# Kernel tuning notes

Measured on AMD Instinct MI355X. Metric: run time of the kernel, lower is better.

## Reference

```python
import jax, jax.numpy as jnp
import numpy as np

B, N, X_DIM, Y_DIM, H_DIM, R_DIM = 64, 512, 128, 128, 4096, 1024


def setup_inputs() -> dict:
    key = jax.random.key(0)
    ks = jax.random.split(key, 10)
    x = jax.random.normal(ks[0], (B, N, X_DIM), dtype=jnp.float32)
    y = jax.random.normal(ks[1], (B, N, Y_DIM), dtype=jnp.float32)
    # per-sample context lengths in [1, N]; prefix mask guarantees >=1 True per row
    lengths = jax.random.randint(ks[2], (B,), 1, N + 1)
    mask = (jnp.arange(N)[None, :] < lengths[:, None])  # [B, N] bool
    d_in = X_DIM + Y_DIM
    s1 = 1.0 / np.sqrt(d_in)
    s2 = 1.0 / np.sqrt(H_DIM)
    W1 = jax.random.uniform(ks[3], (d_in, H_DIM), jnp.float32, -s1, s1)
    b1 = jax.random.uniform(ks[4], (H_DIM,), jnp.float32, -s1, s1)
    W2 = jax.random.uniform(ks[5], (H_DIM, H_DIM), jnp.float32, -s2, s2)
    b2 = jax.random.uniform(ks[6], (H_DIM,), jnp.float32, -s2, s2)
    W3 = jax.random.uniform(ks[7], (H_DIM, R_DIM), jnp.float32, -s2, s2)
    b3 = jax.random.uniform(ks[8], (R_DIM,), jnp.float32, -s2, s2)
    return {"x": x, "y": y, "mask": mask,
            "W1": W1, "b1": b1, "W2": W2, "b2": b2, "W3": W3, "b3": b3}


def reference(x, y, mask, W1, b1, W2, b2, W3, b3):
    # Dense equivalent of gather -> MLP -> scatter_mean by batch id:
    # the MLP is pointwise over tokens, so applying it densely and taking a
    # masked mean over the point dim gives identical math to the ragged path.
    nn_in = jnp.concatenate([x, y], axis=-1)          # [B, N, x+y]
    h = jax.nn.relu(jnp.einsum('bnd,dh->bnh', nn_in, W1) + b1)
    h = jax.nn.relu(jnp.einsum('bnh,hk->bnk', h, W2) + b2)
    r = jnp.einsum('bnk,kr->bnr', h, W3) + b3          # [B, N, r_dim]
    m = mask.astype(r.dtype)[..., None]                # [B, N, 1]
    counts = jnp.maximum(m.sum(axis=1), 1.0)           # [B, 1]
    r_aggr = (r * m).sum(axis=1) / counts              # [B, r_dim]
    return r_aggr
```

## Files before the change

kernel.cpp:

```cpp
#include <hip/hip_runtime.h>


using u16 = unsigned short;
using u8 = unsigned char;
typedef float f32x4 __attribute__((ext_vector_type(4)));
typedef short s16x8 __attribute__((ext_vector_type(8)));
typedef int i32x4 __attribute__((ext_vector_type(4)));

__device__ __forceinline__ u16 f2bf(float f) {
  union { float f; unsigned u; } v; v.f = f;
  unsigned r = (v.u + 0x7fffu + ((v.u >> 16) & 1u)) >> 16;
  return (u16)r;
}


__global__ void count_k(const int* __restrict__ mask, int* __restrict__ lens) {
  int b = blockIdx.x, l = threadIdx.x;
  const int4* row = (const int4*)(mask + (size_t)b * 512);
  int4 v0 = row[l];
  int4 v1 = row[l + 64];
  int s = v0.x + v0.y + v0.z + v0.w + v1.x + v1.y + v1.z + v1.w;
  #pragma unroll
  for (int o = 32; o; o >>= 1) s += __shfl_down(s, o);
  if (l == 0) lens[b] = s;
}

__global__ void meta_k(const int* __restrict__ lens, int* __restrict__ meta) {
  if (threadIdx.x == 0) {
    int acc = 0; meta[0] = 0;
    for (int b = 0; b < 64; ++b) { acc += lens[b]; meta[b + 1] = acc; }
    meta[65] = acc;
    meta[66] = (acc + 127) >> 7;
  }
}

__global__ void tok2b_k(const int* __restrict__ meta, int* __restrict__ tok2b) {
  int i = blockIdx.x * 256 + threadIdx.x;
  int total = meta[65];
  int b = 64;
  if (i < total) {
    int lo = 0, hi = 64;
    while (hi - lo > 1) { int mid = (lo + hi) >> 1; if (meta[mid] <= i) lo = mid; else hi = mid; }
    b = lo;
  }
  tok2b[i] = b;
}

__global__ void build_a(const float* __restrict__ x, const float* __restrict__ y,
                        const int* __restrict__ meta, const int* __restrict__ tok2b,
                        u16* __restrict__ A) {
  int i4 = blockIdx.x * 256 + threadIdx.x;
  int e = i4 * 4;
  int m = e >> 8, c = e & 255;
  int total = meta[65];
  ushort4 o = {0, 0, 0, 0};
  if (m < total) {
    int b = tok2b[m], t = m - meta[b];
    const float* src = (c < 128) ? x + ((size_t)b * 512 + t) * 128 + c
                                 : y + ((size_t)b * 512 + t) * 128 + (c - 128);
    float4 v = *(const float4*)src;
    o.x = f2bf(v.x); o.y = f2bf(v.y); o.z = f2bf(v.z); o.w = f2bf(v.w);
  }
  *(ushort4*)&A[e] = o;
}

__global__ void pack_k(const float* __restrict__ W, u16* __restrict__ P,
                       int N, int NKB) {
  long c = (long)blockIdx.x * 256 + threadIdx.x;
  int lane = c & 63; long r = c >> 6;
  int s = r & 1; int j = (r >> 1) & 3; int wn = (r >> 3) & 1;
  long q = r >> 4;
  int ktb = (int)(q % NKB), nt = (int)(q / NKB);
  int k = ktb * 64 + s * 32 + (lane >> 4) * 8;
  int n = nt * 128 + wn * 64 + j * 16 + (lane & 15);
  ushort o[8];
  #pragma unroll
  for (int e = 0; e < 8; ++e) o[e] = f2bf(W[(size_t)(k + e) * N + n]);
  *(uint4*)&P[c * 8] = *(uint4*)o;
}

__global__ void colmax_k(const float* __restrict__ W, float* __restrict__ cmax) {
  int n = blockIdx.x * 256 + threadIdx.x;
  int k0 = blockIdx.y * 128;
  float m = 0.f;
  for (int k = k0; k < k0 + 128; ++k)
    m = fmaxf(m, fabsf(W[(size_t)k * 4096 + n]));
  atomicMax((int*)&cmax[n], __float_as_int(m));
}

__global__ void pack8_k(const float* __restrict__ W, const float* __restrict__ cmax,
                        char* __restrict__ P) {
  long c = (long)blockIdx.x * 256 + threadIdx.x;
  int lane = c & 63; long r = c >> 6;
  int j = r & 3; int wn = (r >> 2) & 1; long q = r >> 3;
  int ktb = (int)(q & 63), nt = (int)(q >> 6);
  int k = ktb * 64 + (lane >> 4) * 16;
  int n = nt * 128 + wn * 64 + j * 16 + (lane & 15);
  float rw = 127.0f / fmaxf(cmax[n], 1e-20f);
  char o[16];
  #pragma unroll
  for (int e = 0; e < 16; ++e) {
    int v = __float2int_rn(W[(size_t)(k + e) * 4096 + n] * rw);
    v = v > 127 ? 127 : (v < -127 ? -127 : v);
    o[e] = (char)v;
  }
  *(uint4*)&P[c * 16] = *(const uint4*)o;
}

__global__ void sn_k(const float* __restrict__ S, const int* __restrict__ lens,
                     u16* __restrict__ Sn) {
  int i4 = blockIdx.x * 256 + threadIdx.x;
  int e = i4 * 4;
  int m = e >> 12;
  float inv = (m < 64) ? (1.0f / (float)lens[m]) : 0.0f;
  float4 v = *(const float4*)(S + e);
  ushort4 o;
  o.x = f2bf(v.x * inv); o.y = f2bf(v.y * inv);
  o.z = f2bf(v.z * inv); o.w = f2bf(v.w * inv);
  *(ushort4*)&Sn[e] = o;
}

template <int MODE>
__global__ __launch_bounds__(256, 3) void gemm_k(
    const void* __restrict__ Av, int lda, const void* __restrict__ BPv,
    const float* __restrict__ bias, const float* __restrict__ cmax,
    u8* __restrict__ Hout, float* __restrict__ Sout, float* __restrict__ Fout,
    const int* __restrict__ meta, const int* __restrict__ tok2b,
    int K, int Nld, int tile0, int tile_cap) {
  constexpr bool A8 = (MODE == 1);
  constexpr int BK = A8 ? 128 : 64;
  __shared__ union {
    u16 a16[2][128 * 64];
    u8  a8[2][128 * 128];
    u8  outT8[128 * 128];
  } sm;

  const int tid = threadIdx.x;
  const int wave = tid >> 6;
  const int lane = tid & 63;
  const int wm = wave >> 1, wn = wave & 1;
  const int quad = lane >> 4, l15 = lane & 15;
  const int NKB = K >> 6;

  int nslots;
  if constexpr (MODE < 2) {
    int tc = meta[66] - tile0;
    tc = tc < 0 ? 0 : (tc > tile_cap ? tile_cap : tc);
    nslots = tc * 32;
  } else {
    nslots = gridDim.x;
  }

  for (int slot = blockIdx.x; slot < nslots; slot += gridDim.x) {
    int mt, n0, k0, kend;
    if constexpr (MODE < 2) {
      mt = slot >> 5; n0 = (slot & 31) << 7; k0 = 0; kend = K;
    } else {
      mt = 0; n0 = slot << 7; k0 = blockIdx.y * 512; kend = k0 + 512;
    }

    f32x4 accf[4][4];
    i32x4 acci[4][4];
    #pragma unroll
    for (int i = 0; i < 4; i++)
      #pragma unroll
      for (int j = 0; j < 4; j++) {
        if constexpr (A8) acci[i][j] = (i32x4){0, 0, 0, 0};
        else accf[i][j] = (f32x4){0.f, 0.f, 0.f, 0.f};
      }

    const u8* ag8[4];
    const u16* ag16[4];
    if constexpr (A8) {
      #pragma unroll
      for (int il = 0; il < 4; ++il) {
        int ci = (wave * 4 + il) * 64 + lane;
        int m = ci >> 3, c = (ci & 7) ^ (m & 7);
        ag8[il] = (const u8*)Av + (size_t)(mt * 128 + m) * lda + c * 16;
      }
    } else {
      #pragma unroll
      for (int il = 0; il < 4; ++il) {
        int ci = (wave * 4 + il) * 64 + lane;
        int m = ci >> 3, c = (ci & 7) ^ (m & 7);
        ag16[il] = (const u16*)Av + (size_t)(mt * 128 + m) * lda + c * 8;
      }
    }
    const u16* bw = nullptr;
    const u8* bw8 = nullptr;
    if constexpr (A8)
      bw8 = (const u8*)BPv + (size_t)(n0 >> 7) * NKB * 8192 + wn * 4096 + lane * 16;
    else
      bw = (const u16*)BPv + (size_t)(n0 >> 7) * NKB * 8192 + wn * 4096 + lane * 8;

    s16x8 breg0[8], breg1[8];
    i32x4 breg8_0[8], breg8_1[8];

    auto stageA = [&](int kt, int buf) {
      if constexpr (A8) {
        #pragma unroll
        for (int il = 0; il < 4; ++il)
          __builtin_amdgcn_global_load_lds(
              (const __attribute__((address_space(1))) void*)(ag8[il] + kt),
              (__attribute__((address_space(3))) void*)(&sm.a8[buf][(wave * 4 + il) * 1024]),
              16, 0, 0);
      } else {
        #pragma unroll
        for (int il = 0; il < 4; ++il)
          __builtin_amdgcn_global_load_lds(
              (const __attribute__((address_space(1))) void*)(ag16[il] + kt),
              (__attribute__((address_space(3))) void*)(&sm.a16[buf][(wave * 4 + il) * 512]),
              16, 0, 0);
      }
    };
    auto loadB = [&](int kt, int which) {
      if constexpr (A8) {
        i32x4* dst = which ? breg8_1 : breg8_0;
        const u8* p = bw8 + (size_t)(kt >> 6) * 8192;
        #pragma unroll
        for (int s = 0; s < 2; s++)
          #pragma unroll
          for (int j = 0; j < 4; j++)
            dst[s * 4 + j] = *(const i32x4*)(p + s * 8192 + j * 1024);
      } else {
        s16x8* dst = which ? breg1 : breg0;
        const u16* p = bw + (size_t)(kt >> 6) * 8192;
        #pragma unroll
        for (int j = 0; j < 4; j++)
          #pragma unroll
          for (int s = 0; s < 2; s++)
            dst[j * 2 + s] = *(const s16x8*)(p + j * 1024 + s * 512);
      }
    };
    auto compute = [&](int buf) {
      if constexpr (A8) {
        const i32x4* br = buf ? breg8_1 : breg8_0;
        #pragma unroll
        for (int s = 0; s < 2; ++s) {
          #pragma unroll
          for (int i = 0; i < 4; i++) {
            int m = wm * 64 + i * 16 + l15;
            int c = (s * 4 + quad) ^ (m & 7);
            i32x4 a = *(const i32x4*)&sm.a8[buf][(m * 8 + c) * 16];
            #pragma unroll
            for (int j = 0; j < 4; j++)
              acci[i][j] = __builtin_amdgcn_mfma_i32_16x16x64_i8(
                  a, br[s * 4 + j], acci[i][j], 0, 0, 0);
          }
        }
      } else {
        const s16x8* br = buf ? breg1 : breg0;
        #pragma unroll
        for (int s = 0; s < 2; ++s) {
          s16x8 af[4];
          #pragma unroll
          for (int i = 0; i < 4; i++) {
            int m = wm * 64 + i * 16 + l15;
            int c = (s * 4 + quad) ^ (m & 7);
            af[i] = *(const s16x8*)&sm.a16[buf][(m * 8 + c) * 8];
          }
          #pragma unroll
          for (int i = 0; i < 4; i++)
            #pragma unroll
            for (int j = 0; j < 4; j++)
              accf[i][j] = __builtin_amdgcn_mfma_f32_16x16x32_bf16(
                  af[i], br[j * 2 + s], accf[i][j], 0, 0, 0);
        }
      }
    };

    stageA(k0, 0);
    loadB(k0, 0);
    const int NP = (kend - k0) / BK;
    for (int t = 0; t < NP; t += 2) {
      int kt = k0 + t * BK;
      __builtin_amdgcn_s_waitcnt(0x0F78);
      __builtin_amdgcn_s_barrier();
      stageA(kt + BK, 1);
      __builtin_amdgcn_sched_barrier(0);
      loadB(kt + BK, 1);
      compute(0);
      __builtin_amdgcn_s_waitcnt(0x0F78);
      __builtin_amdgcn_s_barrier();
      if (t + 2 < NP) {
        stageA(kt + 2 * BK, 0);
        __builtin_amdgcn_sched_barrier(0);
        loadB(kt + 2 * BK, 0);
      }
      compute(1);
    }
    __syncthreads();

    if constexpr (MODE == 0) {
      float bb[4];
      #pragma unroll
      for (int j = 0; j < 4; j++) bb[j] = bias[n0 + wn * 64 + j * 16 + l15];
      #pragma unroll
      for (int i = 0; i < 4; i++)
        #pragma unroll
        for (int j = 0; j < 4; j++) {
          int col = wn * 64 + j * 16 + l15;
          #pragma unroll
          for (int r = 0; r < 4; r++) {
            int row = wm * 64 + i * 16 + quad * 4 + r;
            float v = accf[i][j][r] + bb[j];
            v = v > 0.f ? v : 0.f;
            int qv = (int)(v * 32.0f + 0.5f);
            if (qv > 127) qv = 127;
            sm.outT8[row * 128 + col] = (u8)qv;
          }
        }
      __syncthreads();
      #pragma unroll
      for (int u = 0; u < 4; ++u) {
        int e = u * 256 + tid;
        int row = e >> 3, c16 = (e & 7) * 16;
        *(uint4*)&Hout[(size_t)(mt * 128 + row) * Nld + n0 + c16] =
            *(const uint4*)&sm.outT8[row * 128 + c16];
      }
      __syncthreads();
    } else if constexpr (MODE == 1) {
      float bb[4], sc[4];
      #pragma unroll
      for (int j = 0; j < 4; j++) {
        int col_ = n0 + wn * 64 + j * 16 + l15;
        bb[j] = bias[col_];
        sc[j] = cmax[col_] * (1.0f / (127.0f * 32.0f));
      }
      int tb[16];
      const int gbase = tile0 * 128 + mt * 128 + wm * 64 + quad * 4;
      #pragma unroll
      for (int i = 0; i < 4; i++)
        #pragma unroll
        for (int r = 0; r < 4; r++) tb[i * 4 + r] = tok2b[gbase + i * 16 + r];
      #pragma unroll
      for (int j = 0; j < 4; j++) {
        int col = n0 + wn * 64 + j * 16 + l15;
        float sum = 0.f;
        int cb = tb[0];
        #pragma unroll
        for (int idx = 0; idx < 16; ++idx) {
          float t = (float)acci[idx >> 2][j][idx & 3] * sc[j] + bb[j];
          t = t > 0.f ? t : 0.f;
          int b = tb[idx];
          if (b != cb) {
            atomicAdd(&Sout[(size_t)cb * 4096 + col], sum);
            sum = 0.f; cb = b;
          }
          sum += t;
        }
        atomicAdd(&Sout[(size_t)cb * 4096 + col], sum);
      }
    } else {
      float bb[4];
      #pragma unroll
      for (int j = 0; j < 4; j++)
        bb[j] = (blockIdx.y == 0) ? bias[n0 + wn * 64 + j * 16 + l15] : 0.f;
      #pragma unroll
      for (int i = 0; i < 4; i++)
        #pragma unroll
        for (int j = 0; j < 4; j++) {
          int col = wn * 64 + j * 16 + l15;
          #pragma unroll
          for (int r = 0; r < 4; r++) {
            int row = wm * 64 + i * 16 + quad * 4 + r;
            if (row < 64)
              atomicAdd(&Fout[(size_t)row * Nld + n0 + col], accf[i][j][r] + bb[j]);
          }
        }
    }
  }
}

extern "C" void kernel_launch(void* const* d_in, const int* in_sizes, int n_in,
                              void* d_out, int out_size, void* d_ws, size_t ws_size,
                              hipStream_t stream) {
  const float* x  = (const float*)d_in[0];
  const float* y  = (const float*)d_in[1];
  const int* mask = (const int*)d_in[2];
  const float* W1 = (const float*)d_in[3];
  const float* b1 = (const float*)d_in[4];
  const float* W2 = (const float*)d_in[5];
  const float* b2 = (const float*)d_in[6];
  const float* W3 = (const float*)d_in[7];
  const float* b3 = (const float*)d_in[8];
  float* out = (float*)d_out;

  char* ws = (char*)d_ws;
  size_t off = 0;
  auto alloc = [&](size_t bytes) {
    char* p = ws + off;
    off += (bytes + 255) & ~(size_t)255;
    return p;
  };
  int* lens  = (int*)alloc(64 * 4);
  int* meta  = (int*)alloc(70 * 4);
  int* tok2b = (int*)alloc((size_t)32768 * 4);
  float* S   = (float*)alloc((size_t)128 * 4096 * 4);
  u16* Sn    = (u16*)alloc((size_t)128 * 4096 * 2);
  float* cm  = (float*)alloc((size_t)4096 * 4);
  u16* W1P   = (u16*)alloc((size_t)256 * 4096 * 2);
  char* W2P8 = (char*)alloc((size_t)4096 * 4096);
  u16* W3P   = (u16*)alloc((size_t)4096 * 1024 * 2);
  u16* Abuf  = (u16*)alloc((size_t)32768 * 256 * 2);
  size_t fixed = off;
  size_t h1_full = (size_t)32768 * 4096;
  int nchunks, tile_cap;
  if (ws_size >= fixed + h1_full) { nchunks = 1; tile_cap = 256; }
  else if (ws_size >= fixed + h1_full / 2) { nchunks = 2; tile_cap = 128; }
  else if (ws_size >= fixed + h1_full / 4) { nchunks = 4; tile_cap = 64; }
  else return;
  u8* H1 = (u8*)alloc(h1_full / nchunks);

  hipMemsetAsync(S, 0, (size_t)128 * 4096 * 4, stream);
  hipMemsetAsync(cm, 0, (size_t)4096 * 4, stream);
  hipMemsetAsync(out, 0, (size_t)out_size * 4, stream);
  count_k<<<64, 64, 0, stream>>>(mask, lens);
  meta_k<<<1, 64, 0, stream>>>(lens, meta);
  tok2b_k<<<128, 256, 0, stream>>>(meta, tok2b);
  build_a<<<8192, 256, 0, stream>>>(x, y, meta, tok2b, Abuf);
  pack_k<<<512, 256, 0, stream>>>(W1, W1P, 4096, 4);
  colmax_k<<<dim3(16, 32), 256, 0, stream>>>(W2, cm);
  pack8_k<<<4096, 256, 0, stream>>>(W2, cm, W2P8);
  pack_k<<<2048, 256, 0, stream>>>(W3, W3P, 1024, 64);

  for (int c = 0; c < nchunks; ++c) {
    gemm_k<0><<<dim3(768), 256, 0, stream>>>(
        Abuf + (size_t)c * tile_cap * 128 * 256, 256, W1P, b1, nullptr, H1,
        nullptr, nullptr, meta, tok2b, 256, 4096, c * tile_cap, tile_cap);
    gemm_k<1><<<dim3(768), 256, 0, stream>>>(
        H1, 4096, W2P8, b2, cm, nullptr, S, nullptr,
        meta, tok2b, 4096, 4096, c * tile_cap, tile_cap);
  }
  sn_k<<<512, 256, 0, stream>>>(S, lens, Sn);
  gemm_k<2><<<dim3(8, 8), 256, 0, stream>>>(
      Sn, 4096, W3P, b3, nullptr, nullptr, nullptr, out,
      meta, tok2b, 4096, 1024, 0, 0);
}
```

Measured before the change: 595.1 us.

## Triple-buffer int8 A tiles in LDS to deepen the GEMM prefetch pipeline

```diff
diff --git a/kernel.cpp b/kernel.cpp
--- a/kernel.cpp
+++ b/kernel.cpp
@@ -131,7 +131,7 @@
   constexpr int BK = A8 ? 128 : 64;
   __shared__ union {
     u16 a16[2][128 * 64];
-    u8  a8[2][128 * 128];
+    u8  a8[3][128 * 128];
     u8  outT8[128 * 128];
   } sm;
 
@@ -232,16 +232,17 @@
             dst[j * 2 + s] = *(const s16x8*)(p + j * 1024 + s * 512);
       }
     };
-    auto compute = [&](int buf) {
+    auto compute = [&](int buf, int which) {
       if constexpr (A8) {
-        const i32x4* br = buf ? breg8_1 : breg8_0;
+        const i32x4* br = which ? breg8_1 : breg8_0;
+        const u8* ab = &sm.a8[0][0] + buf * 16384;
         #pragma unroll
         for (int s = 0; s < 2; ++s) {
           #pragma unroll
           for (int i = 0; i < 4; i++) {
             int m = wm * 64 + i * 16 + l15;
             int c = (s * 4 + quad) ^ (m & 7);
-            i32x4 a = *(const i32x4*)&sm.a8[buf][(m * 8 + c) * 16];
+            i32x4 a = *(const i32x4*)&ab[(m * 8 + c) * 16];
             #pragma unroll
             for (int j = 0; j < 4; j++)
               acci[i][j] = __builtin_amdgcn_mfma_i32_16x16x64_i8(
@@ -249,7 +250,7 @@
           }
         }
       } else {
-        const s16x8* br = buf ? breg1 : breg0;
+        const s16x8* br = which ? breg1 : breg0;
         #pragma unroll
         for (int s = 0; s < 2; ++s) {
           s16x8 af[4];
@@ -269,25 +270,52 @@
       }
     };
 
-    stageA(k0, 0);
-    loadB(k0, 0);
-    const int NP = (kend - k0) / BK;
-    for (int t = 0; t < NP; t += 2) {
-      int kt = k0 + t * BK;
-      __builtin_amdgcn_s_waitcnt(0x0F78);
-      __builtin_amdgcn_s_barrier();
-      stageA(kt + BK, 1);
-      __builtin_amdgcn_sched_barrier(0);
-      loadB(kt + BK, 1);
-      compute(0);
-      __builtin_amdgcn_s_waitcnt(0x0F78);
-      __builtin_amdgcn_s_barrier();
-      if (t + 2 < NP) {
-        stageA(kt + 2 * BK, 0);
+    if constexpr (A8) {
+      stageA(k0, 0);
+      stageA(k0 + BK, 1);
+      loadB(k0, 0);
+      const int NP = (kend - k0) / BK;
+      int bufc = 0, bufs = 2;
+      for (int t = 0; t < NP; t += 2) {
+        int kt = k0 + t * BK;
+        __builtin_amdgcn_s_waitcnt(0x0F7C);
+        __builtin_amdgcn_s_barrier();
+        if (t + 2 < NP) stageA(kt + 2 * BK, bufs);
         __builtin_amdgcn_sched_barrier(0);
-        loadB(kt + 2 * BK, 0);
-      }
-      compute(1);
+        loadB(kt + BK, 1);
+        compute(bufc, 0);
+        bufc = bufc == 2 ? 0 : bufc + 1;
+        bufs = bufs == 2 ? 0 : bufs + 1;
+        __builtin_amdgcn_s_waitcnt(0x0F7C);
+        __builtin_amdgcn_s_barrier();
+        if (t + 3 < NP) stageA(kt + 3 * BK, bufs);
+        __builtin_amdgcn_sched_barrier(0);
+        if (t + 2 < NP) loadB(kt + 2 * BK, 0);
+        compute(bufc, 1);
+        bufc = bufc == 2 ? 0 : bufc + 1;
+        bufs = bufs == 2 ? 0 : bufs + 1;
+      }
+    } else {
+      stageA(k0, 0);
+      loadB(k0, 0);
+      const int NP = (kend - k0) / BK;
+      for (int t = 0; t < NP; t += 2) {
+        int kt = k0 + t * BK;
+        __builtin_amdgcn_s_waitcnt(0x0F78);
+        __builtin_amdgcn_s_barrier();
+        stageA(kt + BK, 1);
+        __builtin_amdgcn_sched_barrier(0);
+        loadB(kt + BK, 1);
+        compute(0, 0);
+        __builtin_amdgcn_s_waitcnt(0x0F78);
+        __builtin_amdgcn_s_barrier();
+        if (t + 2 < NP) {
+          stageA(kt + 2 * BK, 0);
+          __builtin_amdgcn_sched_barrier(0);
+          loadB(kt + 2 * BK, 0);
+        }
+        compute(1, 1);
+      }
     }
     __syncthreads();
 
```

Result: slower. 670.2 us (+12.6%).
